# Performance work log

Measured on AMD Instinct MI355X. Metric: run time of the kernel, lower is better.

Reference implementation:

```python
import jax, jax.numpy as jnp
import numpy as np

BN_EPS = 1e-5

def _mlp_bn(h, W1, b1, g, bt, W2, b2):
    # PyG MLP([d, H, H]): Linear -> BatchNorm (batch stats) -> ReLU -> Linear (plain last)
    h = h @ W1 + b1
    mu = jnp.mean(h, axis=0)
    var = jnp.var(h, axis=0)
    h = (h - mu) * jax.lax.rsqrt(var + BN_EPS) * g + bt
    return jax.nn.relu(h) @ W2 + b2

def _gine(x, src, dst, edge_attr, p):
    # GINEConv, eps=0: nn(x + sum_{j->i} relu(x_j + lin(e_ji)))
    We, be, W1, b1, g, bt, W2, b2 = p
    msg = jax.nn.relu(x[src] + edge_attr @ We + be)      # [E, d]
    aggr = jax.ops.segment_sum(msg, dst, num_segments=x.shape[0])
    return _mlp_bn(x + aggr, W1, b1, g, bt, W2, b2)

def setup_inputs() -> dict:
    key = jax.random.key(0)
    ks = jax.random.split(key, 64)
    N, E, F_IN, H, OUT, B = 40000, 640000, 16, 128, 8, 64
    inp = {}
    inp["x"] = jax.random.normal(ks[0], (N, F_IN), jnp.float32)
    inp["edge_index"] = jax.random.randint(ks[1], (2, E), 0, N)
    inp["edge_attr"] = jax.random.normal(ks[2], (E, 2), jnp.float32)
    inp["batch"] = jnp.sort(jax.random.randint(ks[3], (N,), 0, B))
    inp["batch_size"] = B
    ki = 4
    for l, d in enumerate([F_IN, H, H]):
        inp[f"We{l}"] = 0.1 * jax.random.normal(ks[ki], (2, d), jnp.float32); ki += 1
        inp[f"be{l}"] = jnp.zeros((d,), jnp.float32)
        inp[f"W1{l}"] = 0.1 * jax.random.normal(ks[ki], (d, H), jnp.float32); ki += 1
        inp[f"b1{l}"] = jnp.zeros((H,), jnp.float32)
        inp[f"g{l}"] = jnp.ones((H,), jnp.float32)
        inp[f"bt{l}"] = jnp.zeros((H,), jnp.float32)
        inp[f"W2{l}"] = 0.1 * jax.random.normal(ks[ki], (H, H), jnp.float32); ki += 1
        inp[f"b2{l}"] = jnp.zeros((H,), jnp.float32)
    inp["Wf1"] = 0.1 * jax.random.normal(ks[ki], (H, H), jnp.float32); ki += 1
    inp["bf1"] = jnp.zeros((H,), jnp.float32)
    inp["Wf2"] = 0.1 * jax.random.normal(ks[ki], (H, OUT), jnp.float32); ki += 1
    inp["bf2"] = jnp.zeros((OUT,), jnp.float32)
    return inp

def reference(x, edge_index, edge_attr, batch, batch_size,
              We0, be0, W10, b10, g0, bt0, W20, b20,
              We1, be1, W11, b11, g1, bt1, W21, b21,
              We2, be2, W12, b12, g2, bt2, W22, b22,
              Wf1, bf1, Wf2, bf2):
    src, dst = edge_index[0], edge_index[1]
    layers = [(We0, be0, W10, b10, g0, bt0, W20, b20),
              (We1, be1, W11, b11, g1, bt1, W21, b21),
              (We2, be2, W12, b12, g2, bt2, W22, b22)]
    for p in layers:
        x = jax.nn.relu(_gine(x, src, dst, edge_attr, p))
    pooled = jax.ops.segment_sum(x, batch, num_segments=batch_size)  # global_add_pool [B, H]
    h = jax.nn.relu(pooled @ Wf1 + bf1)  # final MLP, norm=None, dropout eval-mode identity
    return h @ Wf2 + bf2
```

## Files before the change

kernel.cpp:

```cpp
#include <hip/hip_runtime.h>
#include <hip/hip_bf16.h>

#define N_NODES 40000
#define N_EDGES 640000
#define HID 128
#define NB 64
#define F_IN 16
#define BN_EPS 1e-5f
#define SCAN_NBLK ((N_NODES + 255) / 256)
#define NT_ROWS (N_NODES / 16)
#define POOL_ROWS 40
#define POOL_NBLK (N_NODES / POOL_ROWS)

typedef unsigned short u16;
typedef unsigned int u32;
typedef unsigned long long u64;
typedef __attribute__((ext_vector_type(8))) __bf16 bf16x8;
typedef __attribute__((ext_vector_type(8))) unsigned short u16x8;
typedef __attribute__((ext_vector_type(4))) float f32x4;

__device__ __forceinline__ float bf2f(u16 u) {
  u32 v = ((u32)u) << 16;
  return __builtin_bit_cast(float, v);
}
__device__ __forceinline__ u16 f2bf(float f) {
  u32 v = __builtin_bit_cast(u32, f);
  u32 r = 0x7FFFu + ((v >> 16) & 1u);
  return (u16)((v + r) >> 16);
}
__device__ __forceinline__ float pk_hi(u32 p) {
  return __builtin_bit_cast(float, p & 0xFFFF0000u);
}
__device__ __forceinline__ float pk_lo(u32 p) {
  return __builtin_bit_cast(float, p << 16);
}

__global__ __launch_bounds__(256) void hist_kernel(const int* __restrict__ ei,
                                                   int* __restrict__ deg) {
  int e = blockIdx.x * 256 + threadIdx.x;
  if (e < N_EDGES) atomicAdd(&deg[ei[N_EDGES + e]], 1);
}

__global__ __launch_bounds__(256) void scan1(const int* __restrict__ deg,
                                             int* __restrict__ offs,
                                             int* __restrict__ bsum) {
  __shared__ int sh[256];
  int t = threadIdx.x;
  int i = blockIdx.x * 256 + t;
  int v = (i < N_NODES) ? deg[i] : 0;
  sh[t] = v;
  __syncthreads();
#pragma unroll
  for (int off = 1; off < 256; off <<= 1) {
    int u = (t >= off) ? sh[t - off] : 0;
    __syncthreads();
    sh[t] += u;
    __syncthreads();
  }
  if (i < N_NODES) offs[i] = sh[t] - v;
  if (t == 255) bsum[blockIdx.x] = sh[255];
}

__global__ __launch_bounds__(256) void scan2(int* __restrict__ bsum) {
  __shared__ int sh[256];
  int t = threadIdx.x;
  int v = (t < SCAN_NBLK) ? bsum[t] : 0;
  sh[t] = v;
  __syncthreads();
#pragma unroll
  for (int off = 1; off < 256; off <<= 1) {
    int u = (t >= off) ? sh[t - off] : 0;
    __syncthreads();
    sh[t] += u;
    __syncthreads();
  }
  if (t < SCAN_NBLK) bsum[t] = sh[t] - v;
}

__global__ __launch_bounds__(256) void scan3(const int* __restrict__ bsum,
                                             int* __restrict__ offs,
                                             int* __restrict__ cursor) {
  int i = blockIdx.x * 256 + threadIdx.x;
  if (i < N_NODES) {
    int o = offs[i] + bsum[blockIdx.x];
    offs[i] = o;
    cursor[i] = o;
  }
  if (i == 0) offs[N_NODES] = N_EDGES;
}

__global__ __launch_bounds__(256) void scatter_kernel(
    const int* __restrict__ ei, const float* __restrict__ ea,
    int* __restrict__ cursor, uint2* __restrict__ elpk) {
  int e = blockIdx.x * 256 + threadIdx.x;
  if (e >= N_EDGES) return;
  int d = ei[N_EDGES + e];
  int pos = atomicAdd(&cursor[d], 1);
  u32 a0 = (u32)f2bf(ea[2 * e]) << 16;
  u32 a1 = (u32)f2bf(ea[2 * e + 1]);
  u64 rec = (u64)(a0 | a1) << 32 | (u32)ei[e];
  __builtin_nontemporal_store(rec, (u64*)&elpk[pos]);
}

__global__ __launch_bounds__(128) void wconv(const float* __restrict__ W,
                                             u16* __restrict__ Wt) {
  int k = blockIdx.x;
  int n = threadIdx.x;
  Wt[n * HID + k] = f2bf(W[k * HID + n]);
}

__global__ __launch_bounds__(64) void aggregate128_bf16(
    const u16* __restrict__ xb, const int* __restrict__ offs,
    const uint2* __restrict__ elpk, const float* __restrict__ We,
    const float* __restrict__ be, u16* __restrict__ out) {
  int i = blockIdx.x;
  int c = threadIdx.x * 2;
  float2 we0 = *(const float2*)(We + c);
  float2 we1 = *(const float2*)(We + HID + c);
  float2 bec = *(const float2*)(be + c);
  ushort2 xs = *(const ushort2*)(xb + (size_t)i * HID + c);
  float acc0 = bf2f(xs.x), acc1 = bf2f(xs.y);
  int s0 = offs[i], s1 = offs[i + 1];
  int n = s1 - s0;
  int nfull = n & ~3;

#define EDGE(rr, uu)                                                      \
  {                                                                       \
    float a0 = pk_hi((rr).y), a1 = pk_lo((rr).y);                         \
    acc0 += fmaxf(bf2f((uu).x) + a0 * we0.x + a1 * we1.x + bec.x, 0.f);   \
    acc1 += fmaxf(bf2f((uu).y) + a0 * we0.y + a1 * we1.y + bec.y, 0.f);   \
  }

  if (nfull >= 4) {
    uint2 r0 = elpk[s0], r1 = elpk[s0 + 1], r2 = elpk[s0 + 2],
          r3 = elpk[s0 + 3];
    ushort2 u0 = *(const ushort2*)(xb + (size_t)r0.x * HID + c);
    ushort2 u1 = *(const ushort2*)(xb + (size_t)r1.x * HID + c);
    ushort2 u2 = *(const ushort2*)(xb + (size_t)r2.x * HID + c);
    ushort2 u3 = *(const ushort2*)(xb + (size_t)r3.x * HID + c);
    for (int j = s0 + 4; j < s0 + nfull; j += 4) {
      uint2 n0 = elpk[j], n1 = elpk[j + 1], n2 = elpk[j + 2],
            n3 = elpk[j + 3];
      ushort2 v0 = *(const ushort2*)(xb + (size_t)n0.x * HID + c);
      ushort2 v1 = *(const ushort2*)(xb + (size_t)n1.x * HID + c);
      ushort2 v2 = *(const ushort2*)(xb + (size_t)n2.x * HID + c);
      ushort2 v3 = *(const ushort2*)(xb + (size_t)n3.x * HID + c);
      EDGE(r0, u0) EDGE(r1, u1) EDGE(r2, u2) EDGE(r3, u3)
      r0 = n0; u0 = v0; r1 = n1; u1 = v1;
      r2 = n2; u2 = v2; r3 = n3; u3 = v3;
    }
    EDGE(r0, u0) EDGE(r1, u1) EDGE(r2, u2) EDGE(r3, u3)
  }
  for (int j = s0 + nfull; j < s1; j++) {
    uint2 r = elpk[j];
    ushort2 u = *(const ushort2*)(xb + (size_t)r.x * HID + c);
    EDGE(r, u)
  }
#undef EDGE

  ushort2 o;
  o.x = f2bf(acc0);
  o.y = f2bf(acc1);
  *(ushort2*)(out + (size_t)i * HID + c) = o;
}

__global__ __launch_bounds__(128) void aggregate16(
    const float* __restrict__ x, const int* __restrict__ offs,
    const uint2* __restrict__ elpk, const float* __restrict__ We,
    const float* __restrict__ be, float* __restrict__ out) {
  int tid = threadIdx.x;
  int i = blockIdx.x * 8 + (tid >> 4);
  int c = tid & 15;
  float we0 = We[c], we1 = We[F_IN + c], bec = be[c];
  float acc = x[i * F_IN + c];
  int s0 = offs[i], s1 = offs[i + 1];
  for (int j = s0; j < s1; j++) {
    uint2 r = elpk[j];
    float a0 = pk_hi(r.y), a1 = pk_lo(r.y);
    acc += fmaxf(x[r.x * F_IN + c] + a0 * we0 + a1 * we1 + bec, 0.f);
  }
  out[i * F_IN + c] = acc;
}

template <bool PRO, bool STATS, bool RELU>
__global__ __launch_bounds__(256, 2) void gemm_mfma(
    const u16* __restrict__ Ab, const u16* __restrict__ Wt,
    const float* __restrict__ bias, const float* __restrict__ stat_in,
    const float* __restrict__ gg, const float* __restrict__ btp,
    u16* __restrict__ outb, float* __restrict__ stat_out) {
  __shared__ float sc[HID], sh[HID];
  int tid = threadIdx.x;
  int lane = tid & 63;
  int wid = tid >> 6;
  int l15 = lane & 15;
  int quad = lane >> 4;
  int gwave = blockIdx.x * 4 + wid;
  int nwaves = gridDim.x * 4;

  if (PRO) {
    if (tid < HID) {
      float mu = stat_in[tid] * (1.f / N_NODES);
      float var = stat_in[HID + tid] * (1.f / N_NODES) - mu * mu;
      float s = gg[tid] * rsqrtf(var + BN_EPS);
      sc[tid] = s;
      sh[tid] = btp[tid] - mu * s;
    }
    __syncthreads();
  }

  bf16x8 bfr[8][4];
#pragma unroll
  for (int ct = 0; ct < 8; ct++)
#pragma unroll
    for (int ks = 0; ks < 4; ks++)
      bfr[ct][ks] = __builtin_bit_cast(
          bf16x8, *(const u16x8*)(Wt + (size_t)(ct * 16 + l15) * HID +
                                  ks * 32 + quad * 8));

  float bv[8];
#pragma unroll
  for (int ct = 0; ct < 8; ct++) bv[ct] = bias[ct * 16 + l15];

  float s[8], q[8];
  if (STATS) {
#pragma unroll
    for (int ct = 0; ct < 8; ct++) {
      s[ct] = 0.f;
      q[ct] = 0.f;
    }
  }

  for (int t = gwave; t < NT_ROWS; t += nwaves) {
    int r0 = t * 16;
    const u16* arow = Ab + (size_t)(r0 + l15) * HID + quad * 8;
    bf16x8 af[4];
#pragma unroll
    for (int ks = 0; ks < 4; ks++) {
      u16x8 raw = *(const u16x8*)(arow + ks * 32);
      if (PRO) {
        u16x8 pr;
#pragma unroll
        for (int j = 0; j < 8; j++) {
          int k = ks * 32 + quad * 8 + j;
          float v = bf2f(raw[j]);
          v = fmaxf(v * sc[k] + sh[k], 0.f);
          pr[j] = f2bf(v);
        }
        raw = pr;
      }
      af[ks] = __builtin_bit_cast(bf16x8, raw);
    }

    f32x4 acc[8];
#pragma unroll
    for (int ct = 0; ct < 8; ct++) acc[ct] = (f32x4){0.f, 0.f, 0.f, 0.f};
#pragma unroll
    for (int ks = 0; ks < 4; ks++)
#pragma unroll
      for (int ct = 0; ct < 8; ct++)
        acc[ct] = __builtin_amdgcn_mfma_f32_16x16x32_bf16(af[ks], bfr[ct][ks],
                                                          acc[ct], 0, 0, 0);

#pragma unroll
    for (int ct = 0; ct < 8; ct++) {
      u16* op = outb + (size_t)(r0 + quad * 4) * HID + ct * 16 + l15;
#pragma unroll
      for (int r = 0; r < 4; r++) {
        float h = acc[ct][r] + bv[ct];
        if (STATS) {
          s[ct] += h;
          q[ct] += h * h;
        }
        if (RELU) h = fmaxf(h, 0.f);
        op[(size_t)r * HID] = f2bf(h);
      }
    }
  }

  if (STATS) {
    __shared__ float sred[4][256];
#pragma unroll
    for (int ct = 0; ct < 8; ct++) {
      float sv = s[ct], qv = q[ct];
      sv += __shfl_xor(sv, 16);
      sv += __shfl_xor(sv, 32);
      qv += __shfl_xor(qv, 16);
      qv += __shfl_xor(qv, 32);
      if (quad == 0) {
        sred[wid][ct * 16 + l15] = sv;
        sred[wid][128 + ct * 16 + l15] = qv;
      }
    }
    __syncthreads();
    float tot = sred[0][tid] + sred[1][tid] + sred[2][tid] + sred[3][tid];
    atomicAdd(stat_out + tid, tot);
  }
}

__global__ __launch_bounds__(256) void gemm16_f32(
    const float* __restrict__ A, const float* __restrict__ W,
    const float* __restrict__ bias, u16* __restrict__ outb,
    float* __restrict__ stat) {
  constexpr int KT = 16;
  __shared__ float Wl[KT][HID];
  __shared__ float Al[32][KT];
  __shared__ float red[8][2][HID];

  int tid = threadIdx.x;
  int cg = tid & 31;
  int rg = tid >> 5;
  int c = cg << 2;
  int row0 = blockIdx.x * 32;

  float4 acc[4];
#pragma unroll
  for (int i = 0; i < 4; i++) acc[i] = make_float4(0.f, 0.f, 0.f, 0.f);

  for (int i = tid; i < KT * (HID / 4); i += 256) {
    int k = i >> 5;
    int cc = (i & 31) << 2;
    *(float4*)&Wl[k][cc] = *(const float4*)(W + k * HID + cc);
  }
  for (int i = tid; i < 32 * KT / 4; i += 256) {
    int r = i / (KT / 4);
    int k4 = (i % (KT / 4)) << 2;
    *(float4*)&Al[r][k4] = *(const float4*)(A + (size_t)(row0 + r) * KT + k4);
  }
  __syncthreads();
#pragma unroll
  for (int k = 0; k < KT; k++) {
    float4 w4 = *(float4*)&Wl[k][c];
#pragma unroll
    for (int i = 0; i < 4; i++) {
      float a = Al[rg * 4 + i][k];
      acc[i].x += a * w4.x;
      acc[i].y += a * w4.y;
      acc[i].z += a * w4.z;
      acc[i].w += a * w4.w;
    }
  }

  float4 bv = *(const float4*)(bias + c);
  float4 sm = make_float4(0.f, 0.f, 0.f, 0.f);
  float4 qm = make_float4(0.f, 0.f, 0.f, 0.f);
#pragma unroll
  for (int i = 0; i < 4; i++) {
    acc[i].x += bv.x; acc[i].y += bv.y; acc[i].z += bv.z; acc[i].w += bv.w;
    sm.x += acc[i].x; sm.y += acc[i].y; sm.z += acc[i].z; sm.w += acc[i].w;
    qm.x += acc[i].x * acc[i].x; qm.y += acc[i].y * acc[i].y;
    qm.z += acc[i].z * acc[i].z; qm.w += acc[i].w * acc[i].w;
    ushort4 o16;
    o16.x = f2bf(acc[i].x); o16.y = f2bf(acc[i].y);
    o16.z = f2bf(acc[i].z); o16.w = f2bf(acc[i].w);
    *(ushort4*)(outb + (size_t)(row0 + rg * 4 + i) * HID + c) = o16;
  }
  *(float4*)&red[rg][0][c] = sm;
  *(float4*)&red[rg][1][c] = qm;
  __syncthreads();
  if (tid < HID) {
    float sv = 0.f, qv = 0.f;
#pragma unroll
    for (int r = 0; r < 8; r++) {
      sv += red[r][0][tid];
      qv += red[r][1][tid];
    }
    atomicAdd(stat + tid, sv);
    atomicAdd(stat + HID + tid, qv);
  }
}

__global__ __launch_bounds__(64) void pool_kernel(
    const u16* __restrict__ xb, const int* __restrict__ batch,
    float* __restrict__ pooled) {
  int c = threadIdx.x * 2;
  int r0 = blockIdx.x * POOL_ROWS;
  int r1 = r0 + POOL_ROWS;
  if (r1 > N_NODES) r1 = N_NODES;
  float a0 = 0.f, a1 = 0.f;
  int cur = batch[r0];
  for (int r = r0; r < r1; r++) {
    int b = batch[r];
    if (b != cur) {
      atomicAdd(pooled + cur * HID + c, a0);
      atomicAdd(pooled + cur * HID + c + 1, a1);
      a0 = 0.f;
      a1 = 0.f;
      cur = b;
    }
    ushort2 u = *(const ushort2*)(xb + (size_t)r * HID + c);
    a0 += bf2f(u.x);
    a1 += bf2f(u.y);
  }
  atomicAdd(pooled + cur * HID + c, a0);
  atomicAdd(pooled + cur * HID + c + 1, a1);
}

__global__ __launch_bounds__(128) void final_mlp(
    const float* __restrict__ pooled, const float* __restrict__ Wf1,
    const float* __restrict__ bf1, const float* __restrict__ Wf2,
    const float* __restrict__ bf2, float* __restrict__ out) {
  __shared__ float pr[HID];
  __shared__ float h[HID];
  int b = blockIdx.x, c = threadIdx.x;
  pr[c] = pooled[b * HID + c];
  __syncthreads();
  float acc = bf1[c];
  for (int k = 0; k < HID; k++) acc += pr[k] * Wf1[k * HID + c];
  h[c] = fmaxf(acc, 0.f);
  __syncthreads();
  if (c < 8) {
    float o = bf2[c];
    for (int k = 0; k < HID; k++) o += h[k] * Wf2[k * 8 + c];
    out[b * 8 + c] = o;
  }
}

extern "C" void kernel_launch(void* const* d_in, const int* in_sizes, int n_in,
                              void* d_out, int out_size, void* d_ws,
                              size_t ws_size, hipStream_t stream) {
  const float* x_in = (const float*)d_in[0];
  const int* ei = (const int*)d_in[1];
  const float* ea = (const float*)d_in[2];
  const int* batch = (const int*)d_in[3];
  const float* We[3], *be[3], *W1[3], *b1[3], *g[3], *bt[3], *W2[3], *b2[3];
  for (int l = 0; l < 3; l++) {
    int i0 = 5 + 8 * l;
    We[l] = (const float*)d_in[i0 + 0];
    be[l] = (const float*)d_in[i0 + 1];
    W1[l] = (const float*)d_in[i0 + 2];
    b1[l] = (const float*)d_in[i0 + 3];
    g[l] = (const float*)d_in[i0 + 4];
    bt[l] = (const float*)d_in[i0 + 5];
    W2[l] = (const float*)d_in[i0 + 6];
    b2[l] = (const float*)d_in[i0 + 7];
  }
  const float* Wf1 = (const float*)d_in[29];
  const float* bf1 = (const float*)d_in[30];
  const float* Wf2 = (const float*)d_in[31];
  const float* bf2 = (const float*)d_in[32];
  float* out = (float*)d_out;

  const size_t NH = (size_t)N_NODES * HID;
  u16* xb = (u16*)d_ws;
  u16* abuf = xb + NH;
  u16* hbuf = abuf + NH;
  float* agg16 = (float*)(hbuf + NH);
  float* stat0 = agg16 + (size_t)N_NODES * F_IN;
  float* stat1 = stat0 + 256;
  float* stat2 = stat1 + 256;
  float* pooled = stat2 + 256;
  u16* wt[5];
  wt[0] = (u16*)(pooled + NB * HID);
  for (int i = 1; i < 5; i++) wt[i] = wt[i - 1] + HID * HID;
  int* deg = (int*)(wt[4] + HID * HID);
  int* offs = deg + N_NODES;
  int* cursor = offs + N_NODES + 2;
  int* bsum = cursor + N_NODES;
  uint2* elpk = (uint2*)(bsum + 256);
  float* stats[3] = {stat0, stat1, stat2};

  hipMemsetAsync(deg, 0, N_NODES * sizeof(int), stream);
  hipMemsetAsync(stat0, 0, 768 * sizeof(float), stream);
  hipLaunchKernelGGL(hist_kernel, dim3((N_EDGES + 255) / 256), dim3(256), 0,
                     stream, ei, deg);
  hipLaunchKernelGGL(scan1, dim3(SCAN_NBLK), dim3(256), 0, stream, deg, offs,
                     bsum);
  hipLaunchKernelGGL(scan2, dim3(1), dim3(256), 0, stream, bsum);
  hipLaunchKernelGGL(scan3, dim3(SCAN_NBLK), dim3(256), 0, stream, bsum, offs,
                     cursor);
  hipLaunchKernelGGL(scatter_kernel, dim3((N_EDGES + 255) / 256), dim3(256), 0,
                     stream, ei, ea, cursor, elpk);

  hipLaunchKernelGGL(wconv, dim3(HID), dim3(HID), 0, stream, W2[0], wt[0]);
  hipLaunchKernelGGL(wconv, dim3(HID), dim3(HID), 0, stream, W1[1], wt[1]);
  hipLaunchKernelGGL(wconv, dim3(HID), dim3(HID), 0, stream, W2[1], wt[2]);
  hipLaunchKernelGGL(wconv, dim3(HID), dim3(HID), 0, stream, W1[2], wt[3]);
  hipLaunchKernelGGL(wconv, dim3(HID), dim3(HID), 0, stream, W2[2], wt[4]);

  const int GMB = 313;

  hipLaunchKernelGGL(aggregate16, dim3(N_NODES / 8), dim3(128), 0, stream,
                     x_in, offs, elpk, We[0], be[0], agg16);
  hipLaunchKernelGGL(gemm16_f32, dim3(N_NODES / 32), dim3(256), 0, stream,
                     agg16, W1[0], b1[0], hbuf, stat0);
  hipLaunchKernelGGL((gemm_mfma<true, false, true>), dim3(GMB), dim3(256), 0,
                     stream, hbuf, wt[0], b2[0], stat0, g[0], bt[0], xb,
                     nullptr);

  for (int l = 1; l < 3; l++) {
    hipLaunchKernelGGL(aggregate128_bf16, dim3(N_NODES), dim3(64), 0, stream,
                       xb, offs, elpk, We[l], be[l], abuf);
    hipLaunchKernelGGL((gemm_mfma<false, true, false>), dim3(GMB), dim3(256),
                       0, stream, abuf, wt[2 * l - 1], b1[l], nullptr, nullptr,
                       nullptr, hbuf, stats[l]);
    hipLaunchKernelGGL((gemm_mfma<true, false, true>), dim3(GMB), dim3(256), 0,
                       stream, hbuf, wt[2 * l], b2[l], stats[l], g[l], bt[l],
                       xb, nullptr);
  }

  hipMemsetAsync(pooled, 0, (size_t)NB * HID * sizeof(float), stream);
  hipLaunchKernelGGL(pool_kernel, dim3(POOL_NBLK), dim3(64), 0, stream, xb,
                     batch, pooled);
  hipLaunchKernelGGL(final_mlp, dim3(NB), dim3(128), 0, stream, pooled, Wf1,
                     bf1, Wf2, bf2, out);
}
```

Baseline: 440.3 us.

## Build CSR with two-pass shared-memory radix partition instead of global atomics

Replaces the per-edge global-atomic degree histogram, three-kernel scan and atomic scatter with a coarse bucket histogram, a single-block scan, a block-local partition into 157 destination buckets, and a per-bucket fine sort. Almost all counting atomics move to shared memory, and the writes land in more localized regions. The low destination bits are packed into the upper half of the source index, so the gather paths now mask the source with 0xFFFF. This relies on node count staying below 65536 and adds an extra 5 MB intermediate edge buffer to the workspace.

```diff
diff --git a/kernel.cpp b/kernel.cpp
--- a/kernel.cpp
+++ b/kernel.cpp
@@ -7,10 +7,11 @@
 #define NB 64
 #define F_IN 16
 #define BN_EPS 1e-5f
-#define SCAN_NBLK ((N_NODES + 255) / 256)
 #define NT_ROWS (N_NODES / 16)
 #define POOL_ROWS 40
 #define POOL_NBLK (N_NODES / POOL_ROWS)
+#define CB 157
+#define P1B 157
 
 typedef unsigned short u16;
 typedef unsigned int u32;
@@ -35,19 +36,28 @@
   return __builtin_bit_cast(float, p << 16);
 }
 
-__global__ __launch_bounds__(256) void hist_kernel(const int* __restrict__ ei,
-                                                   int* __restrict__ deg) {
-  int e = blockIdx.x * 256 + threadIdx.x;
-  if (e < N_EDGES) atomicAdd(&deg[ei[N_EDGES + e]], 1);
-}
-
-__global__ __launch_bounds__(256) void scan1(const int* __restrict__ deg,
-                                             int* __restrict__ offs,
-                                             int* __restrict__ bsum) {
+__global__ __launch_bounds__(256) void coarse_hist(const int* __restrict__ ei,
+                                                   int* __restrict__ ctot) {
+  __shared__ int h[CB];
+  for (int t = threadIdx.x; t < CB; t += 256) h[t] = 0;
+  __syncthreads();
+  int eb = blockIdx.x * 4096;
+#pragma unroll
+  for (int k = 0; k < 16; k++) {
+    int e = eb + k * 256 + threadIdx.x;
+    if (e < N_EDGES) atomicAdd(&h[ei[N_EDGES + e] >> 8], 1);
+  }
+  __syncthreads();
+  for (int t = threadIdx.x; t < CB; t += 256)
+    if (h[t]) atomicAdd(&ctot[t], h[t]);
+}
+
+__global__ __launch_bounds__(256) void coarse_scan(const int* __restrict__ ctot,
+                                                   int* __restrict__ bstart,
+                                                   int* __restrict__ bcur) {
   __shared__ int sh[256];
   int t = threadIdx.x;
-  int i = blockIdx.x * 256 + t;
-  int v = (i < N_NODES) ? deg[i] : 0;
+  int v = (t < CB) ? ctot[t] : 0;
   sh[t] = v;
   __syncthreads();
 #pragma unroll
@@ -57,49 +67,87 @@
     sh[t] += u;
     __syncthreads();
   }
-  if (i < N_NODES) offs[i] = sh[t] - v;
-  if (t == 255) bsum[blockIdx.x] = sh[255];
-}
-
-__global__ __launch_bounds__(256) void scan2(int* __restrict__ bsum) {
-  __shared__ int sh[256];
-  int t = threadIdx.x;
-  int v = (t < SCAN_NBLK) ? bsum[t] : 0;
-  sh[t] = v;
+  if (t < CB) {
+    int e = sh[t] - v;
+    bstart[t] = e;
+    bcur[t] = e;
+  }
+  if (t == 0) bstart[CB] = N_EDGES;
+}
+
+__global__ __launch_bounds__(256) void partition1(const int* __restrict__ ei,
+                                                  const float* __restrict__ ea,
+                                                  int* __restrict__ bcur,
+                                                  u64* __restrict__ elc) {
+  __shared__ int h[CB], base[CB];
+  for (int t = threadIdx.x; t < CB; t += 256) h[t] = 0;
+  __syncthreads();
+  int eb = blockIdx.x * 4096;
+#pragma unroll
+  for (int k = 0; k < 16; k++) {
+    int e = eb + k * 256 + threadIdx.x;
+    if (e < N_EDGES) atomicAdd(&h[ei[N_EDGES + e] >> 8], 1);
+  }
+  __syncthreads();
+  for (int t = threadIdx.x; t < CB; t += 256) {
+    if (h[t]) base[t] = atomicAdd(&bcur[t], h[t]);
+    h[t] = 0;
+  }
+  __syncthreads();
+#pragma unroll
+  for (int k = 0; k < 16; k++) {
+    int e = eb + k * 256 + threadIdx.x;
+    if (e < N_EDGES) {
+      int d = ei[N_EDGES + e];
+      int b = d >> 8;
+      int r = atomicAdd(&h[b], 1);
+      float2 a = *(const float2*)(ea + 2 * e);
+      u32 hi = ((u32)f2bf(a.x) << 16) | f2bf(a.y);
+      u32 lo = (u32)ei[e] | ((u32)(d & 255) << 16);
+      elc[base[b] + r] = ((u64)hi << 32) | lo;
+    }
+  }
+}
+
+__global__ __launch_bounds__(256) void partition2(const u64* __restrict__ elc,
+                                                  const int* __restrict__ bstart,
+                                                  uint2* __restrict__ elpk,
+                                                  int* __restrict__ offs) {
+  __shared__ int h[256], ex[256];
+  int b = blockIdx.x;
+  int tid = threadIdx.x;
+  int s0 = bstart[b], s1 = bstart[b + 1];
+  h[tid] = 0;
+  __syncthreads();
+  for (int j = s0 + tid; j < s1; j += 256) {
+    u32 lo = (u32)elc[j];
+    atomicAdd(&h[(lo >> 16) & 255], 1);
+  }
+  __syncthreads();
+  ex[tid] = h[tid];
   __syncthreads();
 #pragma unroll
   for (int off = 1; off < 256; off <<= 1) {
-    int u = (t >= off) ? sh[t - off] : 0;
+    int u = (tid >= off) ? ex[tid - off] : 0;
     __syncthreads();
-    sh[t] += u;
+    ex[tid] += u;
     __syncthreads();
   }
-  if (t < SCAN_NBLK) bsum[t] = sh[t] - v;
-}
-
-__global__ __launch_bounds__(256) void scan3(const int* __restrict__ bsum,
-                                             int* __restrict__ offs,
-                                             int* __restrict__ cursor) {
-  int i = blockIdx.x * 256 + threadIdx.x;
-  if (i < N_NODES) {
-    int o = offs[i] + bsum[blockIdx.x];
-    offs[i] = o;
-    cursor[i] = o;
-  }
-  if (i == 0) offs[N_NODES] = N_EDGES;
-}
-
-__global__ __launch_bounds__(256) void scatter_kernel(
-    const int* __restrict__ ei, const float* __restrict__ ea,
-    int* __restrict__ cursor, uint2* __restrict__ elpk) {
-  int e = blockIdx.x * 256 + threadIdx.x;
-  if (e >= N_EDGES) return;
-  int d = ei[N_EDGES + e];
-  int pos = atomicAdd(&cursor[d], 1);
-  u32 a0 = (u32)f2bf(ea[2 * e]) << 16;
-  u32 a1 = (u32)f2bf(ea[2 * e + 1]);
-  u64 rec = (u64)(a0 | a1) << 32 | (u32)ei[e];
-  __builtin_nontemporal_store(rec, (u64*)&elpk[pos]);
+  int excl = ex[tid] - h[tid];
+  int node = b * 256 + tid;
+  if (node < N_NODES) offs[node] = s0 + excl;
+  if (b == 0 && tid == 0) offs[N_NODES] = N_EDGES;
+  h[tid] = s0 + excl;
+  __syncthreads();
+  for (int j = s0 + tid; j < s1; j += 256) {
+    u64 rec = elc[j];
+    int dl = ((u32)rec >> 16) & 255;
+    int pos = atomicAdd(&h[dl], 1);
+    uint2 o;
+    o.x = (u32)rec;
+    o.y = (u32)(rec >> 32);
+    elpk[pos] = o;
+  }
 }
 
 __global__ __launch_bounds__(128) void wconv(const float* __restrict__ W,
@@ -130,21 +178,22 @@
     acc0 += fmaxf(bf2f((uu).x) + a0 * we0.x + a1 * we1.x + bec.x, 0.f);   \
     acc1 += fmaxf(bf2f((uu).y) + a0 * we0.y + a1 * we1.y + bec.y, 0.f);   \
   }
+#define GATHER(rr) *(const ushort2*)(xb + (size_t)((rr).x & 0xFFFFu) * HID + c)
 
   if (nfull >= 4) {
     uint2 r0 = elpk[s0], r1 = elpk[s0 + 1], r2 = elpk[s0 + 2],
           r3 = elpk[s0 + 3];
-    ushort2 u0 = *(const ushort2*)(xb + (size_t)r0.x * HID + c);
-    ushort2 u1 = *(const ushort2*)(xb + (size_t)r1.x * HID + c);
-    ushort2 u2 = *(const ushort2*)(xb + (size_t)r2.x * HID + c);
-    ushort2 u3 = *(const ushort2*)(xb + (size_t)r3.x * HID + c);
+    ushort2 u0 = GATHER(r0);
+    ushort2 u1 = GATHER(r1);
+    ushort2 u2 = GATHER(r2);
+    ushort2 u3 = GATHER(r3);
     for (int j = s0 + 4; j < s0 + nfull; j += 4) {
       uint2 n0 = elpk[j], n1 = elpk[j + 1], n2 = elpk[j + 2],
             n3 = elpk[j + 3];
-      ushort2 v0 = *(const ushort2*)(xb + (size_t)n0.x * HID + c);
-      ushort2 v1 = *(const ushort2*)(xb + (size_t)n1.x * HID + c);
-      ushort2 v2 = *(const ushort2*)(xb + (size_t)n2.x * HID + c);
-      ushort2 v3 = *(const ushort2*)(xb + (size_t)n3.x * HID + c);
+      ushort2 v0 = GATHER(n0);
+      ushort2 v1 = GATHER(n1);
+      ushort2 v2 = GATHER(n2);
+      ushort2 v3 = GATHER(n3);
       EDGE(r0, u0) EDGE(r1, u1) EDGE(r2, u2) EDGE(r3, u3)
       r0 = n0; u0 = v0; r1 = n1; u1 = v1;
       r2 = n2; u2 = v2; r3 = n3; u3 = v3;
@@ -153,9 +202,10 @@
   }
   for (int j = s0 + nfull; j < s1; j++) {
     uint2 r = elpk[j];
-    ushort2 u = *(const ushort2*)(xb + (size_t)r.x * HID + c);
+    ushort2 u = GATHER(r);
     EDGE(r, u)
   }
+#undef GATHER
 #undef EDGE
 
   ushort2 o;
@@ -177,7 +227,8 @@
   for (int j = s0; j < s1; j++) {
     uint2 r = elpk[j];
     float a0 = pk_hi(r.y), a1 = pk_lo(r.y);
-    acc += fmaxf(x[r.x * F_IN + c] + a0 * we0 + a1 * we1 + bec, 0.f);
+    acc += fmaxf(x[(r.x & 0xFFFFu) * F_IN + c] + a0 * we0 + a1 * we1 + bec,
+                 0.f);
   }
   out[i * F_IN + c] = acc;
 }
@@ -452,24 +503,23 @@
   u16* wt[5];
   wt[0] = (u16*)(pooled + NB * HID);
   for (int i = 1; i < 5; i++) wt[i] = wt[i - 1] + HID * HID;
-  int* deg = (int*)(wt[4] + HID * HID);
-  int* offs = deg + N_NODES;
-  int* cursor = offs + N_NODES + 2;
-  int* bsum = cursor + N_NODES;
-  uint2* elpk = (uint2*)(bsum + 256);
+  int* ctot = (int*)(wt[4] + HID * HID);
+  int* bstart = ctot + 160;
+  int* bcur = bstart + 160;
+  int* offs = bcur + 160;
+  u64* elc = (u64*)(offs + 40002);
+  uint2* elpk = (uint2*)(elc + N_EDGES);
   float* stats[3] = {stat0, stat1, stat2};
 
-  hipMemsetAsync(deg, 0, N_NODES * sizeof(int), stream);
+  hipMemsetAsync(ctot, 0, CB * sizeof(int), stream);
   hipMemsetAsync(stat0, 0, 768 * sizeof(float), stream);
-  hipLaunchKernelGGL(hist_kernel, dim3((N_EDGES + 255) / 256), dim3(256), 0,
-                     stream, ei, deg);
-  hipLaunchKernelGGL(scan1, dim3(SCAN_NBLK), dim3(256), 0, stream, deg, offs,
-                     bsum);
-  hipLaunchKernelGGL(scan2, dim3(1), dim3(256), 0, stream, bsum);
-  hipLaunchKernelGGL(scan3, dim3(SCAN_NBLK), dim3(256), 0, stream, bsum, offs,
-                     cursor);
-  hipLaunchKernelGGL(scatter_kernel, dim3((N_EDGES + 255) / 256), dim3(256), 0,
-                     stream, ei, ea, cursor, elpk);
+  hipLaunchKernelGGL(coarse_hist, dim3(P1B), dim3(256), 0, stream, ei, ctot);
+  hipLaunchKernelGGL(coarse_scan, dim3(1), dim3(256), 0, stream, ctot, bstart,
+                     bcur);
+  hipLaunchKernelGGL(partition1, dim3(P1B), dim3(256), 0, stream, ei, ea, bcur,
+                     elc);
+  hipLaunchKernelGGL(partition2, dim3(CB), dim3(256), 0, stream, elc, bstart,
+                     elpk, offs);
 
   hipLaunchKernelGGL(wconv, dim3(HID), dim3(HID), 0, stream, W2[0], wt[0]);
   hipLaunchKernelGGL(wconv, dim3(HID), dim3(HID), 0, stream, W1[1], wt[1]);
```

Result: faster. 386.8 us (-12.2%).
